# Kernel tuning notes

Measured on AMD Instinct MI355X. Metric: run time of the kernel, lower is better.

Reference implementation:

```python
import jax, jax.numpy as jnp
import numpy as np

N_CELLS = 50000
DEG = 32
NNZ = N_CELLS * DEG
D_IN = 64
D_OUT = 64
NEG_SLOPE = 0.2


def setup_inputs() -> dict:
    key = jax.random.key(0)
    k0, k1, k2, k3, k4 = jax.random.split(key, 5)
    x_source = jax.random.normal(k0, (N_CELLS, D_IN), jnp.float32)
    # COO indices of the sparse neighborhood matrix N: DEG entries per row
    edge_rows = jnp.repeat(jnp.arange(N_CELLS, dtype=jnp.int32), DEG)
    edge_cols = jax.random.randint(k1, (NNZ,), 0, N_CELLS, dtype=jnp.int32)
    neighborhood_values = jax.random.uniform(k2, (NNZ,), jnp.float32)
    # xavier_uniform-ish scales (exact init irrelevant for correctness baseline)
    W0 = jax.random.normal(k3, (D_IN, D_OUT), jnp.float32) * (1.414 / np.sqrt(D_IN))
    a0 = jax.random.normal(k4, (2 * D_OUT, 1), jnp.float32) * 0.1
    return {
        "x_source": x_source,
        "edge_rows": edge_rows,
        "edge_cols": edge_cols,
        "neighborhood_values": neighborhood_values,
        "W0": W0,
        "a0": a0,
    }


def reference(x_source, edge_rows, edge_cols, neighborhood_values, W0, a0):
    # message = X W_p  : [n_cells, d_out]
    message = x_source @ W0
    d = message.shape[1]
    # [X_i || X_j] a  ==  (X_i a_src) + (X_j a_dst); compute node-level dot first,
    # then gather per edge (avoids materializing [nnz, 2d] concat)
    a_src = a0[:d, 0]
    a_dst = a0[d:, 0]
    node_src = message @ a_src  # [n_cells]
    node_dst = message @ a_dst  # [n_cells]
    e = jax.nn.leaky_relu(node_src[edge_rows] + node_dst[edge_cols],
                          negative_slope=NEG_SLOPE)  # [nnz]
    # sparse_row_norm: divide each edge value by its row sum (softmax=False path)
    row_sum = jax.ops.segment_sum(e, edge_rows, num_segments=N_CELLS)
    att = e / row_sum[edge_rows]
    # Hadamard product N^1 \odot A_1, then SpMM with message
    vals = neighborhood_values * att  # [nnz]
    out = jax.ops.segment_sum(vals[:, None] * message[edge_cols], edge_rows,
                              num_segments=N_CELLS)  # [n_cells, d_out]
    # update_func='relu'
    return jax.nn.relu(out)
```

## Files before the change

### kernel.cpp

```cpp
#include <hip/hip_runtime.h>
#include <hip/hip_fp16.h>

#define N_CELLS 50000
#define DEG 32
#define DIM 64
#define NEG_SLOPE 0.2

__global__ __launch_bounds__(256)
void gat_prep(const float* __restrict__ x,
              const float* __restrict__ W0,
              const float* __restrict__ a0,
              __half* __restrict__ x2,
              double* __restrict__ ns,
              double* __restrict__ nd) {
  __shared__ double2 p_s[DIM];

  const int tid = threadIdx.x;
  if (tid < DIM) {
    double ps = 0.0, pd = 0.0;
    const float4* w4 = (const float4*)(W0 + tid * DIM);
#pragma unroll
    for (int q = 0; q < DIM / 4; ++q) {
      float4 w = w4[q];
      ps = fma((double)w.x, (double)a0[4 * q + 0], ps);
      ps = fma((double)w.y, (double)a0[4 * q + 1], ps);
      ps = fma((double)w.z, (double)a0[4 * q + 2], ps);
      ps = fma((double)w.w, (double)a0[4 * q + 3], ps);
      pd = fma((double)w.x, (double)a0[DIM + 4 * q + 0], pd);
      pd = fma((double)w.y, (double)a0[DIM + 4 * q + 1], pd);
      pd = fma((double)w.z, (double)a0[DIM + 4 * q + 2], pd);
      pd = fma((double)w.w, (double)a0[DIM + 4 * q + 3], pd);
    }
    p_s[tid] = make_double2(ps, pd);
  }
  __syncthreads();

  const int gtid = blockIdx.x * 256 + tid;
  const int nthreads = gridDim.x * 256;

  const float2* xf2 = (const float2*)x;
  __half2* xh2 = (__half2*)x2;
  for (int i = gtid; i < N_CELLS * DIM / 2; i += nthreads) {
    float2 v = xf2[i];
    xh2[i] = __float22half2_rn(v);
  }

  for (int r = gtid; r < N_CELLS; r += nthreads) {
    const float4* x4 = (const float4*)(x + (size_t)r * DIM);
    double s0 = 0.0, s1 = 0.0, d0 = 0.0, d1 = 0.0;
#pragma unroll
    for (int q = 0; q < DIM / 4; ++q) {
      float4 v = x4[q];
      double2 p0 = p_s[4 * q + 0], p1 = p_s[4 * q + 1];
      double2 p2 = p_s[4 * q + 2], p3 = p_s[4 * q + 3];
      s0 = fma((double)v.x, p0.x, s0); d0 = fma((double)v.x, p0.y, d0);
      s1 = fma((double)v.y, p1.x, s1); d1 = fma((double)v.y, p1.y, d1);
      s0 = fma((double)v.z, p2.x, s0); d0 = fma((double)v.z, p2.y, d0);
      s1 = fma((double)v.w, p3.x, s1); d1 = fma((double)v.w, p3.y, d1);
    }
    ns[r] = s0 + s1;
    nd[r] = d0 + d1;
  }
}

__global__ __launch_bounds__(256)
void gat_edges(const __half* __restrict__ x2,
               const int* __restrict__ ecol,
               const float* __restrict__ nv,
               const float* __restrict__ W0,
               const double* __restrict__ ns,
               const double* __restrict__ nd,
               float* __restrict__ out) {
  __shared__ __align__(16) float w_s[4][2][DEG];
  __shared__ __align__(16) int c_s[4][2][DEG];
  __shared__ __align__(16) float h_s[4][2][DIM];

  const int lane = threadIdx.x & 63;
  const int wid = threadIdx.x >> 6;
  const int half = lane >> 5;
  const int sub = lane & 31;

  float w0c[DIM];
#pragma unroll
  for (int k = 0; k < DIM; ++k) w0c[k] = W0[k * DIM + lane];

  const int gwave = blockIdx.x * 4 + wid;
  const int nwaves = gridDim.x * 4;
  const int npairs = N_CELLS / 2;

  for (int p = gwave; p < npairs; p += nwaves) {
    const int r0 = 2 * p;
    const int myrow = r0 + half;

    const int eidx = r0 * DEG + lane;
    const int col = ecol[eidx];
    const float nvv = nv[eidx];
    double z = ns[myrow] + nd[col];
    double e = (z >= 0.0) ? z : NEG_SLOPE * z;
    double rs = e;
#pragma unroll
    for (int m = 16; m >= 1; m >>= 1) rs += __shfl_xor(rs, m, 64);
    w_s[wid][half][sub] = (float)((double)nvv * (e / rs));
    c_s[wid][half][sub] = col;

    const unsigned* xp = (const unsigned*)x2;
    float ax = 0.0f, ay = 0.0f;
#pragma unroll
    for (int j = 0; j < DEG; ++j) {
      int c = c_s[wid][half][j];
      float w = w_s[wid][half][j];
      unsigned pk = xp[(size_t)c * (DIM / 2) + sub];
      float2 xv = __half22float2(*(const __half2*)&pk);
      ax = fmaf(w, xv.x, ax);
      ay = fmaf(w, xv.y, ay);
    }
    ((float2*)h_s[wid][half])[sub] = make_float2(ax, ay);

    float oA = 0.0f, oB = 0.0f;
    const float4* hA = (const float4*)h_s[wid][0];
    const float4* hB = (const float4*)h_s[wid][1];
#pragma unroll
    for (int q = 0; q < DIM / 4; ++q) {
      float4 a = hA[q];
      float4 b = hB[q];
      oA = fmaf(a.x, w0c[4 * q + 0], oA); oB = fmaf(b.x, w0c[4 * q + 0], oB);
      oA = fmaf(a.y, w0c[4 * q + 1], oA); oB = fmaf(b.y, w0c[4 * q + 1], oB);
      oA = fmaf(a.z, w0c[4 * q + 2], oA); oB = fmaf(b.z, w0c[4 * q + 2], oB);
      oA = fmaf(a.w, w0c[4 * q + 3], oA); oB = fmaf(b.w, w0c[4 * q + 3], oB);
    }
    out[(size_t)r0 * DIM + lane] = fmaxf(oA, 0.0f);
    out[(size_t)(r0 + 1) * DIM + lane] = fmaxf(oB, 0.0f);
  }
}

extern "C" void kernel_launch(void* const* d_in, const int* in_sizes, int n_in,
                              void* d_out, int out_size, void* d_ws, size_t ws_size,
                              hipStream_t stream) {
  const float* x = (const float*)d_in[0];
  const int* ecol = (const int*)d_in[2];
  const float* nv = (const float*)d_in[3];
  const float* W0 = (const float*)d_in[4];
  const float* a0 = (const float*)d_in[5];
  float* out = (float*)d_out;

  __half* x2 = (__half*)d_ws;
  double* ns = (double*)((char*)d_ws + (size_t)N_CELLS * DIM * sizeof(__half));
  double* nd = ns + N_CELLS;

  hipLaunchKernelGGL(gat_prep, dim3(512), dim3(256), 0, stream,
                     x, W0, a0, x2, ns, nd);
  hipLaunchKernelGGL(gat_edges, dim3(2500), dim3(256), 0, stream,
                     x2, ecol, nv, W0, ns, nd, out);
}
```

Baseline: 127.5 us.

## Fuse fp16 conversion into row prep, batch gathers, double-buffer scratch, nontemporal IO

The prep kernel now gives each thread one row. It reads that row once, using it both for the attention dots and for the fp16 conversion, instead of sweeping x twice. The edge kernel issues 8 independent gathers per batch with vectorized LDS reads of columns and weights, and double-buffers the per-wave h_s scratch. It also uses nontemporal loads and stores for streaming data, sets launch_bounds occupancy to 4, and shrinks the grid to 1280 blocks. The per-thread row writes of 128 bytes in prep are strided, so global stores coalesce poorly, and occupancy hints may raise register pressure given the 64-float w0c array.

```diff
diff --git a/kernel.cpp b/kernel.cpp
--- a/kernel.cpp
+++ b/kernel.cpp
@@ -5,6 +5,7 @@
 #define DEG 32
 #define DIM 64
 #define NEG_SLOPE 0.2
+#define NPAIRS (N_CELLS / 2)
 
 __global__ __launch_bounds__(256)
 void gat_prep(const float* __restrict__ x,
@@ -35,35 +36,34 @@
   }
   __syncthreads();
 
-  const int gtid = blockIdx.x * 256 + tid;
-  const int nthreads = gridDim.x * 256;
+  const int r = blockIdx.x * 256 + tid;
+  if (r >= N_CELLS) return;
 
-  const float2* xf2 = (const float2*)x;
-  __half2* xh2 = (__half2*)x2;
-  for (int i = gtid; i < N_CELLS * DIM / 2; i += nthreads) {
-    float2 v = xf2[i];
-    xh2[i] = __float22half2_rn(v);
+  const float4* x4 = (const float4*)(x + (size_t)r * DIM);
+  double s0 = 0.0, s1 = 0.0, d0 = 0.0, d1 = 0.0;
+  __half2 hbuf[DIM / 2];
+#pragma unroll
+  for (int q = 0; q < DIM / 4; ++q) {
+    float4 v = x4[q];
+    double2 p0 = p_s[4 * q + 0], p1 = p_s[4 * q + 1];
+    double2 p2 = p_s[4 * q + 2], p3 = p_s[4 * q + 3];
+    s0 = fma((double)v.x, p0.x, s0); d0 = fma((double)v.x, p0.y, d0);
+    s1 = fma((double)v.y, p1.x, s1); d1 = fma((double)v.y, p1.y, d1);
+    s0 = fma((double)v.z, p2.x, s0); d0 = fma((double)v.z, p2.y, d0);
+    s1 = fma((double)v.w, p3.x, s1); d1 = fma((double)v.w, p3.y, d1);
+    hbuf[2 * q + 0] = __float22half2_rn(make_float2(v.x, v.y));
+    hbuf[2 * q + 1] = __float22half2_rn(make_float2(v.z, v.w));
   }
+  ns[r] = s0 + s1;
+  nd[r] = d0 + d1;
 
-  for (int r = gtid; r < N_CELLS; r += nthreads) {
-    const float4* x4 = (const float4*)(x + (size_t)r * DIM);
-    double s0 = 0.0, s1 = 0.0, d0 = 0.0, d1 = 0.0;
+  const uint4* src = (const uint4*)hbuf;
+  uint4* p2v = (uint4*)(x2 + (size_t)r * DIM);
 #pragma unroll
-    for (int q = 0; q < DIM / 4; ++q) {
-      float4 v = x4[q];
-      double2 p0 = p_s[4 * q + 0], p1 = p_s[4 * q + 1];
-      double2 p2 = p_s[4 * q + 2], p3 = p_s[4 * q + 3];
-      s0 = fma((double)v.x, p0.x, s0); d0 = fma((double)v.x, p0.y, d0);
-      s1 = fma((double)v.y, p1.x, s1); d1 = fma((double)v.y, p1.y, d1);
-      s0 = fma((double)v.z, p2.x, s0); d0 = fma((double)v.z, p2.y, d0);
-      s1 = fma((double)v.w, p3.x, s1); d1 = fma((double)v.w, p3.y, d1);
-    }
-    ns[r] = s0 + s1;
-    nd[r] = d0 + d1;
-  }
+  for (int i = 0; i < 8; ++i) p2v[i] = src[i];
 }
 
-__global__ __launch_bounds__(256)
+__global__ __launch_bounds__(256, 4)
 void gat_edges(const __half* __restrict__ x2,
                const int* __restrict__ ecol,
                const float* __restrict__ nv,
@@ -73,7 +73,7 @@
                float* __restrict__ out) {
   __shared__ __align__(16) float w_s[4][2][DEG];
   __shared__ __align__(16) int c_s[4][2][DEG];
-  __shared__ __align__(16) float h_s[4][2][DIM];
+  __shared__ __align__(16) float h_s[4][2][2][DIM];
 
   const int lane = threadIdx.x & 63;
   const int wid = threadIdx.x >> 6;
@@ -86,16 +86,16 @@
 
   const int gwave = blockIdx.x * 4 + wid;
   const int nwaves = gridDim.x * 4;
-  const int npairs = N_CELLS / 2;
+  const unsigned* xp = (const unsigned*)x2;
 
-  for (int p = gwave; p < npairs; p += nwaves) {
+  int buf = 0;
+  for (int p = gwave; p < NPAIRS; p += nwaves, buf ^= 1) {
     const int r0 = 2 * p;
-    const int myrow = r0 + half;
 
     const int eidx = r0 * DEG + lane;
-    const int col = ecol[eidx];
-    const float nvv = nv[eidx];
-    double z = ns[myrow] + nd[col];
+    const int col = __builtin_nontemporal_load(ecol + eidx);
+    const float nvv = __builtin_nontemporal_load(nv + eidx);
+    double z = ns[r0 + half] + nd[col];
     double e = (z >= 0.0) ? z : NEG_SLOPE * z;
     double rs = e;
 #pragma unroll
@@ -103,22 +103,45 @@
     w_s[wid][half][sub] = (float)((double)nvv * (e / rs));
     c_s[wid][half][sub] = col;
 
-    const unsigned* xp = (const unsigned*)x2;
+    const int* cs = c_s[wid][half];
+    const float* wsp = w_s[wid][half];
     float ax = 0.0f, ay = 0.0f;
 #pragma unroll
-    for (int j = 0; j < DEG; ++j) {
-      int c = c_s[wid][half][j];
-      float w = w_s[wid][half][j];
-      unsigned pk = xp[(size_t)c * (DIM / 2) + sub];
-      float2 xv = __half22float2(*(const __half2*)&pk);
-      ax = fmaf(w, xv.x, ax);
-      ay = fmaf(w, xv.y, ay);
+    for (int q0 = 0; q0 < DEG; q0 += 8) {
+      const int4 ca = ((const int4*)(cs + q0))[0];
+      const int4 cb = ((const int4*)(cs + q0))[1];
+      const float4 wa = ((const float4*)(wsp + q0))[0];
+      const float4 wb = ((const float4*)(wsp + q0))[1];
+      unsigned pk0 = xp[(size_t)ca.x * (DIM / 2) + sub];
+      unsigned pk1 = xp[(size_t)ca.y * (DIM / 2) + sub];
+      unsigned pk2 = xp[(size_t)ca.z * (DIM / 2) + sub];
+      unsigned pk3 = xp[(size_t)ca.w * (DIM / 2) + sub];
+      unsigned pk4 = xp[(size_t)cb.x * (DIM / 2) + sub];
+      unsigned pk5 = xp[(size_t)cb.y * (DIM / 2) + sub];
+      unsigned pk6 = xp[(size_t)cb.z * (DIM / 2) + sub];
+      unsigned pk7 = xp[(size_t)cb.w * (DIM / 2) + sub];
+      float2 v0 = __half22float2(*(const __half2*)&pk0);
+      float2 v1 = __half22float2(*(const __half2*)&pk1);
+      float2 v2 = __half22float2(*(const __half2*)&pk2);
+      float2 v3 = __half22float2(*(const __half2*)&pk3);
+      float2 v4 = __half22float2(*(const __half2*)&pk4);
+      float2 v5 = __half22float2(*(const __half2*)&pk5);
+      float2 v6 = __half22float2(*(const __half2*)&pk6);
+      float2 v7 = __half22float2(*(const __half2*)&pk7);
+      ax = fmaf(wa.x, v0.x, ax); ay = fmaf(wa.x, v0.y, ay);
+      ax = fmaf(wa.y, v1.x, ax); ay = fmaf(wa.y, v1.y, ay);
+      ax = fmaf(wa.z, v2.x, ax); ay = fmaf(wa.z, v2.y, ay);
+      ax = fmaf(wa.w, v3.x, ax); ay = fmaf(wa.w, v3.y, ay);
+      ax = fmaf(wb.x, v4.x, ax); ay = fmaf(wb.x, v4.y, ay);
+      ax = fmaf(wb.y, v5.x, ax); ay = fmaf(wb.y, v5.y, ay);
+      ax = fmaf(wb.z, v6.x, ax); ay = fmaf(wb.z, v6.y, ay);
+      ax = fmaf(wb.w, v7.x, ax); ay = fmaf(wb.w, v7.y, ay);
     }
-    ((float2*)h_s[wid][half])[sub] = make_float2(ax, ay);
+    ((float2*)h_s[wid][buf][half])[sub] = make_float2(ax, ay);
 
     float oA = 0.0f, oB = 0.0f;
-    const float4* hA = (const float4*)h_s[wid][0];
-    const float4* hB = (const float4*)h_s[wid][1];
+    const float4* hA = (const float4*)h_s[wid][buf][0];
+    const float4* hB = (const float4*)h_s[wid][buf][1];
 #pragma unroll
     for (int q = 0; q < DIM / 4; ++q) {
       float4 a = hA[q];
@@ -128,8 +151,8 @@
       oA = fmaf(a.z, w0c[4 * q + 2], oA); oB = fmaf(b.z, w0c[4 * q + 2], oB);
       oA = fmaf(a.w, w0c[4 * q + 3], oA); oB = fmaf(b.w, w0c[4 * q + 3], oB);
     }
-    out[(size_t)r0 * DIM + lane] = fmaxf(oA, 0.0f);
-    out[(size_t)(r0 + 1) * DIM + lane] = fmaxf(oB, 0.0f);
+    __builtin_nontemporal_store(fmaxf(oA, 0.0f), out + (size_t)r0 * DIM + lane);
+    __builtin_nontemporal_store(fmaxf(oB, 0.0f), out + (size_t)(r0 + 1) * DIM + lane);
   }
 }
 
@@ -147,8 +170,8 @@
   double* ns = (double*)((char*)d_ws + (size_t)N_CELLS * DIM * sizeof(__half));
   double* nd = ns + N_CELLS;
 
-  hipLaunchKernelGGL(gat_prep, dim3(512), dim3(256), 0, stream,
+  hipLaunchKernelGGL(gat_prep, dim3((N_CELLS + 255) / 256), dim3(256), 0, stream,
                      x, W0, a0, x2, ns, nd);
-  hipLaunchKernelGGL(gat_edges, dim3(2500), dim3(256), 0, stream,
+  hipLaunchKernelGGL(gat_edges, dim3(1280), dim3(256), 0, stream,
                      x2, ecol, nv, W0, ns, nd, out);
 }
```

New measurement: 123.3 us. 1.03x faster.
